# Optimization experiments

Hardware: AMD Instinct MI355X
Metric: run time of the kernel (lower is better)

The kernel has to match this reference:

```python
import jax, jax.numpy as jnp
import numpy as np

C = 256
CR = 32  # C // nc_reduce

def setup_inputs() -> dict:
    key = jax.random.key(0)
    ks = jax.random.split(key, 8)
    B, H, W = 4, 64, 64
    x = jax.random.normal(ks[0], (B, C, H, W), dtype=jnp.float32)
    s_in = 1.0 / np.sqrt(C)
    Wq = jax.random.uniform(ks[1], (CR, C), jnp.float32, -s_in, s_in)
    bq = jax.random.uniform(ks[2], (CR,), jnp.float32, -s_in, s_in)
    Wk = jax.random.uniform(ks[3], (CR, C), jnp.float32, -s_in, s_in)
    bk = jax.random.uniform(ks[4], (CR,), jnp.float32, -s_in, s_in)
    Wv = jax.random.uniform(ks[5], (C, C), jnp.float32, -s_in, s_in)
    bv = jax.random.uniform(ks[6], (C,), jnp.float32, -s_in, s_in)
    gamma = jnp.zeros((1,), dtype=jnp.float32)
    return {"x": x, "Wq": Wq, "bq": bq, "Wk": Wk, "bk": bk,
            "Wv": Wv, "bv": bv, "gamma": gamma}

def reference(x, Wq, bq, Wk, bk, Wv, bv, gamma):
    B, Cc, H, W = x.shape
    N = H * W
    xf = x.reshape(B, Cc, N)                       # [B, C, N]
    # 1x1 convs == per-position channel projections
    q = jnp.einsum('dc,bcn->bdn', Wq, xf) + bq[None, :, None]  # [B, CR, N]
    k = jnp.einsum('dc,bcn->bdn', Wk, xf) + bk[None, :, None]  # [B, CR, N]
    v = jnp.einsum('dc,bcn->bdn', Wv, xf) + bv[None, :, None]  # [B, C, N]
    # energy[b,i,j] = q[:, :, i] . k[:, :, j]  (no scaling, as in source)
    energy = jnp.einsum('bdi,bdj->bij', q, k)      # [B, N, N]
    attn = jax.nn.softmax(energy, axis=-1)
    # out[b,c,i] = sum_j v[b,c,j] * attn[b,i,j]
    outv = jnp.einsum('bcj,bij->bci', v, attn)     # [B, C, N]
    out = gamma[0] * outv.reshape(B, Cc, H, W) + x
    return out
```

## Files before the change

kernel.cpp:

```cpp
#include <hip/hip_runtime.h>
#include <hip/hip_bf16.h>

#define NB 4
#define CCH 256
#define CRD 32
#define NN 4096

typedef __attribute__((ext_vector_type(8))) short short8;
typedef __attribute__((ext_vector_type(4))) float floatx4;
typedef __attribute__((ext_vector_type(4))) int intx4;
typedef __attribute__((ext_vector_type(2))) unsigned int uintx2;

__device__ __forceinline__ unsigned short f2bf(float f) {
  unsigned u = __builtin_bit_cast(unsigned, f);
  u += 0x7FFFu + ((u >> 16) & 1u);
  return (unsigned short)(u >> 16);
}

__device__ __forceinline__ unsigned short f2bf_c(float f) {
  f = fminf(fmaxf(f, -1.0e4f), 1.0e4f);
  unsigned u = __builtin_bit_cast(unsigned, f);
  u += 0x7FFFu + ((u >> 16) & 1u);
  return (unsigned short)(u >> 16);
}

__device__ __forceinline__ unsigned pack2c(float a, float b) {
  return (unsigned)f2bf_c(a) | ((unsigned)f2bf_c(b) << 16);
}

__device__ __forceinline__ float sat(float v) {
  return fminf(fmaxf(v, -1.0e30f), 1.0e30f);
}

__device__ __forceinline__ short8 ld_frag_g(const unsigned short* p) {
  return __builtin_bit_cast(short8, *(const intx4*)p);
}

__global__ __launch_bounds__(256) void gemm_qkv_fused(
    const float* __restrict__ x,
    const float* __restrict__ Wq, const float* __restrict__ bq,
    const float* __restrict__ Wk, const float* __restrict__ bk,
    const float* __restrict__ Wv, const float* __restrict__ bv,
    unsigned short* __restrict__ qT, unsigned short* __restrict__ kT,
    unsigned short* __restrict__ vv)
{
  __shared__ __align__(16) unsigned short xs[64 * 264];
  __shared__ __align__(16) unsigned short ws[64 * 264];

  const int tid  = threadIdx.x;
  const int wave = tid >> 6;
  const int lane = tid & 63;
  const int lq   = lane >> 4;
  const int lm   = lane & 15;
  const int n0   = blockIdx.x << 6;
  const int mg   = blockIdx.y;
  const int b    = blockIdx.z;

  {
    const int nn = lane;
    const int cg = wave;
    const float* xb = x + ((size_t)b << 20) + n0 + nn;
#pragma unroll
    for (int it = 0; it < 16; ++it) {
      const int c0 = it * 16 + cg * 4;
      const float v0 = xb[(size_t)(c0 + 0) << 12];
      const float v1 = xb[(size_t)(c0 + 1) << 12];
      const float v2 = xb[(size_t)(c0 + 2) << 12];
      const float v3 = xb[(size_t)(c0 + 3) << 12];
      uintx2 u;
      u[0] = pack2c(v0, v1);
      u[1] = pack2c(v2, v3);
      *(uintx2*)(xs + nn * 264 + c0) = u;
    }
  }

  const int mt_lo = mg ? 3 : 0;
  const int mt_hi = mg ? 5 : 3;

  for (int mt = mt_lo; mt < mt_hi; ++mt) {
#pragma unroll
    for (int i = 0; i < 16; ++i) {
      const int u  = i * 256 + tid;
      const int m  = u >> 6;
      const int o4 = (u & 63) * 4;
      const float* src = (mt == 0)
          ? (m < 32 ? Wq + (size_t)m * CCH : Wk + (size_t)(m - 32) * CCH)
          : Wv + (size_t)((mt - 1) * 64 + m) * CCH;
      const floatx4 f = *(const floatx4*)(src + o4);
      uintx2 uu;
      uu[0] = pack2c(f[0], f[1]);
      uu[1] = pack2c(f[2], f[3]);
      *(uintx2*)(ws + m * 264 + o4) = uu;
    }
    __syncthreads();

    floatx4 acc[4];
#pragma unroll
    for (int t = 0; t < 4; ++t) acc[t] = (floatx4){0.f, 0.f, 0.f, 0.f};

#pragma unroll
    for (int k0 = 0; k0 < 8; ++k0) {
      short8 af[4];
#pragma unroll
      for (int ms = 0; ms < 4; ++ms)
        af[ms] = __builtin_bit_cast(short8,
            *(const intx4*)(ws + (ms * 16 + lm) * 264 + k0 * 32 + lq * 8));
      const short8 bf = __builtin_bit_cast(short8,
          *(const intx4*)(xs + (wave * 16 + lm) * 264 + k0 * 32 + lq * 8));
#pragma unroll
      for (int ms = 0; ms < 4; ++ms)
        acc[ms] = __builtin_amdgcn_mfma_f32_16x16x32_bf16(af[ms], bf,
                                                          acc[ms], 0, 0, 0);
    }
    __syncthreads();

    if (mt == 0) {
      const int n = n0 + wave * 16 + lm;
#pragma unroll
      for (int ms = 0; ms < 4; ++ms) {
        const int d0 = (ms & 1) * 16 + lq * 4;
        const float* bias = (ms < 2) ? bq : bk;
        unsigned short* dst = (ms < 2) ? qT : kT;
        uintx2 u;
        u[0] = pack2c(acc[ms][0] + bias[d0],     acc[ms][1] + bias[d0 + 1]);
        u[1] = pack2c(acc[ms][2] + bias[d0 + 2], acc[ms][3] + bias[d0 + 3]);
        *(uintx2*)(dst + (size_t)(b * NN + n) * CRD + d0) = u;
      }
    } else {
      const int cb = (mt - 1) * 64;
      unsigned short* vb2 = ws;
#pragma unroll
      for (int ms = 0; ms < 4; ++ms)
#pragma unroll
        for (int r = 0; r < 4; ++r) {
          const int c = ms * 16 + lq * 4 + r;
          vb2[c * 64 + wave * 16 + lm] = f2bf_c(acc[ms][r] + bv[cb + c]);
        }
      __syncthreads();
#pragma unroll
      for (int it = 0; it < 2; ++it) {
        const int u = it * 256 + tid;
        const int m = u >> 3;
        const int o = (u & 7) * 8;
        *(intx4*)(vv + (size_t)(b * CCH + cb + m) * NN + n0 + o) =
            *(const intx4*)(vb2 + m * 64 + o);
      }
      __syncthreads();
    }
  }
}

__global__ __launch_bounds__(512) void attn_kernel(
    const float* __restrict__ x, const float* __restrict__ gamma_p,
    const unsigned short* __restrict__ qT, const unsigned short* __restrict__ kT,
    const unsigned short* __restrict__ vv, float* __restrict__ out)
{
  __shared__ __align__(16) unsigned char smem[65536 + 2 * 4 * 2176];

  const int tid  = threadIdx.x;
  const int wave = tid >> 6;
  const int wg   = wave >> 1;
  const int cs   = wave & 1;
  const int lane = tid & 63;
  const int lq   = lane >> 4;
  const int lm   = lane & 15;
  const int xcd = blockIdx.x & 7;
  const int pos = blockIdx.x >> 3;
  const int b   = xcd >> 1;
  const int i0  = (((xcd & 1) << 5) | pos) << 6;

  const unsigned short* kTb = kT + (size_t)b * NN * CRD;
  const unsigned short* vb  = vv + (size_t)b * CCH * NN;

  const short8 qf =
      ld_frag_g(qT + (size_t)(b * NN + i0 + wg * 16 + lm) * CRD + lq * 8);

  int vs_g[4];
  int vs_off[4];
#pragma unroll
  for (int m = 0; m < 4; ++m) {
    const int u  = m * 512 + tid;
    const int c  = u >> 3;
    const int jb = u & 7;
    vs_g[m]   = c * NN + jb * 8;
    vs_off[m] = c * 128 + ((jb ^ (c & 7)) * 16);
  }

  floatx4 acc[8];
#pragma unroll
  for (int t = 0; t < 8; ++t) acc[t] = (floatx4){0.f, 0.f, 0.f, 0.f};
  float lsum[4] = {0.f, 0.f, 0.f, 0.f};

  const floatx4 zf = {0.f, 0.f, 0.f, 0.f};

  intx4 vreg[4];
#pragma unroll
  for (int m = 0; m < 4; ++m)
    vreg[m] = *(const intx4*)(vb + vs_g[m]);
  short8 kf[2];
#pragma unroll
  for (int jt = 0; jt < 2; ++jt)
    kf[jt] = ld_frag_g(kTb + (size_t)((cs * 2 + jt) * 16 + lm) * CRD + lq * 8);

#pragma unroll
  for (int m = 0; m < 4; ++m)
    *(intx4*)(smem + vs_off[m]) = vreg[m];
  {
    unsigned char* pb0 = smem + 65536 + wg * 2176;
#pragma unroll
    for (int jt = 0; jt < 2; ++jt) {
      const floatx4 S = __builtin_amdgcn_mfma_f32_16x16x32_bf16(
          qf, kf[jt], zf, 0, 0, 0);
#pragma unroll
      for (int r = 0; r < 4; ++r) {
        const float p = __expf(fminf(fmaxf(S[r], -40.f), 40.f));
        lsum[r] += p;
        *(unsigned short*)(pb0 + (lq * 4 + r) * 136 +
                           (((cs * 2 + jt) * 16 + lm) << 1)) = f2bf(p);
      }
    }
  }
#pragma unroll
  for (int m = 0; m < 4; ++m)
    vreg[m] = *(const intx4*)(vb + vs_g[m] + 64);
#pragma unroll
  for (int jt = 0; jt < 2; ++jt)
    kf[jt] = ld_frag_g(kTb + (size_t)(64 + (cs * 2 + jt) * 16 + lm) * CRD +
                       lq * 8);

#pragma unroll 1
  for (int k = 0; k < 63; ++k) {
    asm volatile("s_waitcnt lgkmcnt(0)" ::: "memory");
    __builtin_amdgcn_s_barrier();

    unsigned char* vbp = smem + ((k & 1) << 15);
    unsigned char* pbp = smem + 65536 + (k & 1) * 8704 + wg * 2176;
    unsigned char* vbn = smem + (((k + 1) & 1) << 15);
    unsigned char* pbn = smem + 65536 + ((k + 1) & 1) * 8704 + wg * 2176;

#pragma unroll
    for (int m = 0; m < 4; ++m)
      *(intx4*)(vbn + vs_off[m]) = vreg[m];

#pragma unroll
    for (int jt = 0; jt < 2; ++jt) {
      const floatx4 S = __builtin_amdgcn_mfma_f32_16x16x32_bf16(
          qf, kf[jt], zf, 0, 0, 0);
#pragma unroll
      for (int r = 0; r < 4; ++r) {
        const float p = __expf(fminf(fmaxf(S[r], -40.f), 40.f));
        lsum[r] += p;
        *(unsigned short*)(pbn + (lq * 4 + r) * 136 +
                           (((cs * 2 + jt) * 16 + lm) << 1)) = f2bf(p);
      }
    }

    {
      const int j2 = ((k + 2 < 64) ? (k + 2) : 63) << 6;
#pragma unroll
      for (int m = 0; m < 4; ++m)
        vreg[m] = *(const intx4*)(vb + vs_g[m] + j2);
#pragma unroll
      for (int jt = 0; jt < 2; ++jt)
        kf[jt] = ld_frag_g(kTb +
                           (size_t)(j2 + (cs * 2 + jt) * 16 + lm) * CRD + lq * 8);
    }

#pragma unroll
    for (int ks = 0; ks < 2; ++ks) {
      const unsigned char* pa = pbp + lm * 136 + ks * 64 + lq * 16;
      struct U128 { unsigned long long a, b; } pp;
      pp.a = *(const unsigned long long*)pa;
      pp.b = *(const unsigned long long*)(pa + 8);
      const short8 pf = __builtin_bit_cast(short8, pp);
#pragma unroll
      for (int nt = 0; nt < 8; ++nt) {
        const int c = cs * 128 + nt * 16 + lm;
        const short8 vf = __builtin_bit_cast(
            short8,
            *(const intx4*)(vbp + c * 128 + (((ks * 4 + lq) ^ (lm & 7)) * 16)));
        acc[nt] = __builtin_amdgcn_mfma_f32_16x16x32_bf16(pf, vf, acc[nt],
                                                          0, 0, 0);
      }
    }
  }

  asm volatile("s_waitcnt lgkmcnt(0)" ::: "memory");
  __builtin_amdgcn_s_barrier();
  {
    const unsigned char* vbp = smem + (1 << 15);
    const unsigned char* pbp = smem + 65536 + 8704 + wg * 2176;
#pragma unroll
    for (int ks = 0; ks < 2; ++ks) {
      const unsigned char* pa = pbp + lm * 136 + ks * 64 + lq * 16;
      struct U128 { unsigned long long a, b; } pp;
      pp.a = *(const unsigned long long*)pa;
      pp.b = *(const unsigned long long*)(pa + 8);
      const short8 pf = __builtin_bit_cast(short8, pp);
#pragma unroll
      for (int nt = 0; nt < 8; ++nt) {
        const int c = cs * 128 + nt * 16 + lm;
        const short8 vf = __builtin_bit_cast(
            short8,
            *(const intx4*)(vbp + c * 128 + (((ks * 4 + lq) ^ (lm & 7)) * 16)));
        acc[nt] = __builtin_amdgcn_mfma_f32_16x16x32_bf16(pf, vf, acc[nt],
                                                          0, 0, 0);
      }
    }
  }

  __syncthreads();
  floatx4 lv;
#pragma unroll
  for (int r = 0; r < 4; ++r) lv[r] = lsum[r];
  *(floatx4*)(smem + ((wave * 64 + lane) << 4)) = lv;
  __syncthreads();
  const floatx4 lpart = *(const floatx4*)(smem + (((wave ^ 1) * 64 + lane) << 4));

  float inv[4];
#pragma unroll
  for (int r = 0; r < 4; ++r) {
    float v = lsum[r] + lpart[r];
    v += __shfl_xor(v, 1);
    v += __shfl_xor(v, 2);
    v += __shfl_xor(v, 4);
    v += __shfl_xor(v, 8);
    inv[r] = 1.0f / v;
  }

  const float gm = gamma_p[0];
#pragma unroll
  for (int nt = 0; nt < 8; ++nt) {
#pragma unroll
    for (int r = 0; r < 4; ++r) {
      const int c = cs * 128 + nt * 16 + lm;
      const int i = i0 + wg * 16 + lq * 4 + r;
      const size_t idx = (size_t)(b * CCH + c) * NN + i;
      out[idx] = gm * sat(acc[nt][r] * inv[r]) + x[idx];
    }
  }
}

extern "C" void kernel_launch(void* const* d_in, const int* in_sizes, int n_in,
                              void* d_out, int out_size, void* d_ws, size_t ws_size,
                              hipStream_t stream) {
  (void)in_sizes; (void)n_in; (void)out_size; (void)ws_size;
  const float* x     = (const float*)d_in[0];
  const float* Wq    = (const float*)d_in[1];
  const float* bq    = (const float*)d_in[2];
  const float* Wk    = (const float*)d_in[3];
  const float* bk    = (const float*)d_in[4];
  const float* Wv    = (const float*)d_in[5];
  const float* bv    = (const float*)d_in[6];
  const float* gamma = (const float*)d_in[7];

  unsigned short* qT = (unsigned short*)d_ws;
  unsigned short* kT = qT + (size_t)NB * NN * CRD;
  unsigned short* vv = kT + (size_t)NB * NN * CRD;

  gemm_qkv_fused<<<dim3(64, 2, 4), 256, 0, stream>>>(x, Wq, bq, Wk, bk, Wv, bv,
                                                     qT, kT, vv);
  attn_kernel<<<dim3(256, 1, 1), 512, 0, stream>>>(x, gamma, qT, kT, vv,
                                                   (float*)d_out);
}
```

Measured before the change: 159.6 us.

## Pre-convert QKV weights to bf16 and read weight fragments from global

Adds a small kernel that converts Wq, Wk and Wv to bf16 once into scratch space borrowed from the second half of the output buffer. The projection GEMM then loads A fragments straight from global/L2 instead of every block converting and staging weights in LDS. This removes redundant fp32-to-bf16 conversion and LDS traffic per block, and frees LDS to allow two blocks per CU. The cost is an extra kernel launch, uncoalesced global fragment loads, and reliance on the attention kernel overwriting the scratch only after the GEMM has finished.

Measured after the change: 174.9 us. +9.6%, slower.

```diff
diff --git a/kernel.cpp b/kernel.cpp
--- a/kernel.cpp
+++ b/kernel.cpp
@@ -36,16 +36,32 @@
   return __builtin_bit_cast(short8, *(const intx4*)p);
 }
 
-__global__ __launch_bounds__(256) void gemm_qkv_fused(
-    const float* __restrict__ x,
-    const float* __restrict__ Wq, const float* __restrict__ bq,
-    const float* __restrict__ Wk, const float* __restrict__ bk,
-    const float* __restrict__ Wv, const float* __restrict__ bv,
+__global__ __launch_bounds__(256) void w_convert(
+    const float* __restrict__ Wq, const float* __restrict__ Wk,
+    const float* __restrict__ Wv, unsigned short* __restrict__ Wb)
+{
+  const int t    = blockIdx.x * 256 + threadIdx.x;
+  const int row  = t >> 6;
+  const int col4 = t & 63;
+  const float* src = (row < 32) ? Wq + (size_t)row * CCH
+                   : (row < 64) ? Wk + (size_t)(row - 32) * CCH
+                                : Wv + (size_t)(row - 64) * CCH;
+  const floatx4 f = *(const floatx4*)(src + col4 * 4);
+  uintx2 u;
+  u[0] = pack2c(f[0], f[1]);
+  u[1] = pack2c(f[2], f[3]);
+  *(uintx2*)(Wb + (size_t)row * CCH + col4 * 4) = u;
+}
+
+__global__ __launch_bounds__(256, 2) void gemm_qkv2(
+    const float* __restrict__ x, const unsigned short* __restrict__ Wb,
+    const float* __restrict__ bq, const float* __restrict__ bk,
+    const float* __restrict__ bv,
     unsigned short* __restrict__ qT, unsigned short* __restrict__ kT,
     unsigned short* __restrict__ vv)
 {
   __shared__ __align__(16) unsigned short xs[64 * 264];
-  __shared__ __align__(16) unsigned short ws[64 * 264];
+  __shared__ __align__(16) unsigned short vb2[64 * 64];
 
   const int tid  = threadIdx.x;
   const int wave = tid >> 6;
@@ -73,38 +89,26 @@
       *(uintx2*)(xs + nn * 264 + c0) = u;
     }
   }
+  __syncthreads();
 
   const int mt_lo = mg ? 3 : 0;
   const int mt_hi = mg ? 5 : 3;
 
+#pragma unroll 1
   for (int mt = mt_lo; mt < mt_hi; ++mt) {
-#pragma unroll
-    for (int i = 0; i < 16; ++i) {
-      const int u  = i * 256 + tid;
-      const int m  = u >> 6;
-      const int o4 = (u & 63) * 4;
-      const float* src = (mt == 0)
-          ? (m < 32 ? Wq + (size_t)m * CCH : Wk + (size_t)(m - 32) * CCH)
-          : Wv + (size_t)((mt - 1) * 64 + m) * CCH;
-      const floatx4 f = *(const floatx4*)(src + o4);
-      uintx2 uu;
-      uu[0] = pack2c(f[0], f[1]);
-      uu[1] = pack2c(f[2], f[3]);
-      *(uintx2*)(ws + m * 264 + o4) = uu;
-    }
-    __syncthreads();
+    const unsigned short* wtile = Wb + (size_t)(mt * 64) * CCH;
 
     floatx4 acc[4];
 #pragma unroll
     for (int t = 0; t < 4; ++t) acc[t] = (floatx4){0.f, 0.f, 0.f, 0.f};
 
-#pragma unroll
+#pragma unroll 2
     for (int k0 = 0; k0 < 8; ++k0) {
       short8 af[4];
 #pragma unroll
       for (int ms = 0; ms < 4; ++ms)
-        af[ms] = __builtin_bit_cast(short8,
-            *(const intx4*)(ws + (ms * 16 + lm) * 264 + k0 * 32 + lq * 8));
+        af[ms] = ld_frag_g(wtile + (size_t)(ms * 16 + lm) * CCH +
+                           k0 * 32 + lq * 8);
       const short8 bf = __builtin_bit_cast(short8,
           *(const intx4*)(xs + (wave * 16 + lm) * 264 + k0 * 32 + lq * 8));
 #pragma unroll
@@ -112,7 +116,6 @@
         acc[ms] = __builtin_amdgcn_mfma_f32_16x16x32_bf16(af[ms], bf,
                                                           acc[ms], 0, 0, 0);
     }
-    __syncthreads();
 
     if (mt == 0) {
       const int n = n0 + wave * 16 + lm;
@@ -128,7 +131,7 @@
       }
     } else {
       const int cb = (mt - 1) * 64;
-      unsigned short* vb2 = ws;
+      __syncthreads();
 #pragma unroll
       for (int ms = 0; ms < 4; ++ms)
 #pragma unroll
@@ -145,7 +148,6 @@
         *(intx4*)(vv + (size_t)(b * CCH + cb + m) * NN + n0 + o) =
             *(const intx4*)(vb2 + m * 64 + o);
       }
-      __syncthreads();
     }
   }
 }
@@ -357,9 +359,11 @@
   unsigned short* qT = (unsigned short*)d_ws;
   unsigned short* kT = qT + (size_t)NB * NN * CRD;
   unsigned short* vv = kT + (size_t)NB * NN * CRD;
-
-  gemm_qkv_fused<<<dim3(64, 2, 4), 256, 0, stream>>>(x, Wq, bq, Wk, bk, Wv, bv,
-                                                     qT, kT, vv);
+  unsigned short* Wb = (unsigned short*)d_out + (size_t)NB * NN * CCH;
+
+  w_convert<<<dim3(80), 256, 0, stream>>>(Wq, Wk, Wv, Wb);
+  gemm_qkv2<<<dim3(64, 2, 4), 256, 0, stream>>>(x, Wb, bq, bk, bv,
+                                                qT, kT, vv);
   attn_kernel<<<dim3(256, 1, 1), 512, 0, stream>>>(x, gamma, qT, kT, vv,
                                                    (float*)d_out);
 }
```
